# Performance work log

Hardware: AMD Instinct MI355X
Metric: run time of the kernel (lower is better)

Reference implementation:

```python
import jax, jax.numpy as jnp
import numpy as np

IN_F = 4096
OUT_F = 4096
B, S = 4, 2048
RMS_EPS = 1e-6
Q_EPS = 1e-5


def setup_inputs() -> dict:
    key = jax.random.key(0)
    kx, kw, kb, ks = jax.random.split(key, 4)
    x = jax.random.normal(kx, (B, S, IN_F), dtype=jnp.float32)
    # ternary BitNet weight in {-1, 0, +1}, stored as float32 for the reference
    W = (jax.random.randint(kw, (OUT_F, IN_F), 0, 3) - 1).astype(jnp.float32)
    rms_weight = jnp.ones((IN_F,), dtype=jnp.float32)
    bias = jax.random.normal(kb, (OUT_F,), dtype=jnp.float32)
    weight_scale = jax.random.uniform(ks, (1,), dtype=jnp.float32) + 0.5
    return {"x": x, "W": W, "rms_weight": rms_weight, "bias": bias,
            "weight_scale": weight_scale}


def reference(x, W, rms_weight, bias, weight_scale):
    # RMSNorm (self.rms_norm applied before quantized matmul)
    var = jnp.mean(x * x, axis=-1, keepdims=True)
    h = x * jax.lax.rsqrt(var + RMS_EPS) * rms_weight
    # BitNet act_quant: per-token absmax int8 quantization
    scale = 127.0 / jnp.clip(jnp.max(jnp.abs(h), axis=-1, keepdims=True), Q_EPS)  # [B,S,1]
    q = jnp.clip(jnp.round(h * scale), -128.0, 127.0)
    # ternary GEMV per token, then dequant
    y = jnp.einsum('bsk,ok->bso', q, W) / scale  # [B,S,OUT_F]
    y = y + bias
    y = y * weight_scale  # weight_scale_mode == 'multiply'
    return y
```

## Files before the change

kernel.cpp:

```cpp
#include <hip/hip_runtime.h>

#define IN_F 4096
#define OUT_F 4096
#define NTOK 8192
#define KDIM 4096

using i32x4 = __attribute__((ext_vector_type(4))) int;
using f32x4 = __attribute__((ext_vector_type(4))) float;

__device__ __forceinline__ void gload_lds16(const void* g, void* l) {
  __builtin_amdgcn_global_load_lds(
      (const __attribute__((address_space(1))) void*)g,
      (__attribute__((address_space(3))) void*)l, 16, 0, 0);
}

#define WAITV(n) asm volatile("s_waitcnt vmcnt(" #n ")" ::: "memory")
#define BAR() do { asm volatile("" ::: "memory"); __builtin_amdgcn_s_barrier(); \
                   asm volatile("" ::: "memory"); } while (0)

__global__ __launch_bounds__(256) void rmsq_kernel(
    const float* __restrict__ x, const float* __restrict__ rmsw,
    signed char* __restrict__ q, float* __restrict__ dscale) {
  const int tok = blockIdx.x;
  const int tid = threadIdx.x;
  const f32x4* xr = (const f32x4*)(x + (size_t)tok * IN_F);
  const f32x4* wr = (const f32x4*)rmsw;

  f32x4 v[4];
  float ss = 0.f;
#pragma unroll
  for (int c = 0; c < 4; ++c) {
    v[c] = xr[c * 256 + tid];
    ss += v[c].x * v[c].x + v[c].y * v[c].y + v[c].z * v[c].z + v[c].w * v[c].w;
  }

  __shared__ float red[4];
#pragma unroll
  for (int off = 32; off > 0; off >>= 1) ss += __shfl_down(ss, off, 64);
  const int wid = tid >> 6;
  if ((tid & 63) == 0) red[wid] = ss;
  __syncthreads();
  const float tot = red[0] + red[1] + red[2] + red[3];
  const float rinv = rsqrtf(tot * (1.0f / IN_F) + 1e-6f);

  f32x4 h[4];
  float amax = 0.f;
#pragma unroll
  for (int c = 0; c < 4; ++c) {
    f32x4 w = wr[c * 256 + tid];
    h[c].x = v[c].x * rinv * w.x;
    h[c].y = v[c].y * rinv * w.y;
    h[c].z = v[c].z * rinv * w.z;
    h[c].w = v[c].w * rinv * w.w;
    amax = fmaxf(amax, fabsf(h[c].x));
    amax = fmaxf(amax, fabsf(h[c].y));
    amax = fmaxf(amax, fabsf(h[c].z));
    amax = fmaxf(amax, fabsf(h[c].w));
  }

  __syncthreads();
#pragma unroll
  for (int off = 32; off > 0; off >>= 1)
    amax = fmaxf(amax, __shfl_down(amax, off, 64));
  if ((tid & 63) == 0) red[wid] = amax;
  __syncthreads();
  amax = fmaxf(fmaxf(red[0], red[1]), fmaxf(red[2], red[3]));
  amax = fmaxf(amax, 1e-5f);
  const float qs = 127.0f / amax;
  if (tid == 0) dscale[tok] = amax * (1.0f / 127.0f);

  uint* qo = (uint*)(q + (size_t)tok * IN_F);
#pragma unroll
  for (int c = 0; c < 4; ++c) {
    float r0 = fminf(fmaxf(rintf(h[c].x * qs), -128.f), 127.f);
    float r1 = fminf(fmaxf(rintf(h[c].y * qs), -128.f), 127.f);
    float r2 = fminf(fmaxf(rintf(h[c].z * qs), -128.f), 127.f);
    float r3 = fminf(fmaxf(rintf(h[c].w * qs), -128.f), 127.f);
    uint p = ((uint)((int)r0 & 255)) | ((uint)((int)r1 & 255) << 8) |
             ((uint)((int)r2 & 255) << 16) | ((uint)((int)r3 & 255) << 24);
    qo[c * 256 + tid] = p;
  }
}

__global__ __launch_bounds__(256) void wconv_kernel(
    const float* __restrict__ W, signed char* __restrict__ Wq) {
  const int idx = blockIdx.x * 256 + threadIdx.x;
  f32x4 w = ((const f32x4*)W)[idx];
  uint p = ((uint)((int)w.x & 255)) | ((uint)((int)w.y & 255) << 8) |
           ((uint)((int)w.z & 255) << 16) | ((uint)((int)w.w & 255) << 24);
  ((uint*)Wq)[idx] = p;
}

#define BM 256
#define BN 256
#define BK 64
#define NT (KDIM / BK)
#define TILEB (BM * BK)
#define BUFB (2 * TILEB)
#define NBUF 4

__global__ __launch_bounds__(512, 2) void gemm_kernel(
    const signed char* __restrict__ A, const signed char* __restrict__ Bw,
    const float* __restrict__ dscale, const float* __restrict__ bias,
    const float* __restrict__ wscale_p, float* __restrict__ out) {
  __shared__ __align__(16) signed char lds[NBUF * BUFB];

  const int tid = threadIdx.x;
  const int lane = tid & 63;
  const int wid = tid >> 6;
  const int wr = wid >> 2;
  const int wc = wid & 3;

  const int bid = blockIdx.x;
  const int swz = (bid & 7) * 64 + (bid >> 3);
  const int m0 = (swz & 31) * BM;
  const int n0 = (swz >> 5) * BN;

  const int cA0 = tid, cA1 = tid + 512;
  const int rA0 = cA0 >> 2, rA1 = cA1 >> 2;
  const int sA0 = (cA0 & 3) ^ ((rA0 >> 1) & 3);
  const int sA1 = (cA1 & 3) ^ ((rA1 >> 1) & 3);
  const signed char* agp0 = A + (size_t)(m0 + rA0) * KDIM + sA0 * 16;
  const signed char* agp1 = A + (size_t)(m0 + rA1) * KDIM + sA1 * 16;
  const signed char* bgp0 = Bw + (size_t)(n0 + rA0) * KDIM + sA0 * 16;
  const signed char* bgp1 = Bw + (size_t)(n0 + rA1) * KDIM + sA1 * 16;

#define STAGE_ALL(kt, bufoff)                                              \
  do {                                                                     \
    const int k0_ = (kt) * BK;                                             \
    signed char* lb_ = &lds[(bufoff)];                                     \
    gload_lds16(agp0 + k0_, lb_ + cA0 * 16);                               \
    gload_lds16(agp1 + k0_, lb_ + cA1 * 16);                               \
    gload_lds16(bgp0 + k0_, lb_ + TILEB + cA0 * 16);                       \
    gload_lds16(bgp1 + k0_, lb_ + TILEB + cA1 * 16);                       \
  } while (0)

  const int fr = lane & 15;
  const int ks = lane >> 4;
  int offA[8], offB[4];
#pragma unroll
  for (int mi = 0; mi < 8; ++mi) {
    const int row = wr * 128 + mi * 16 + fr;
    offA[mi] = row * BK + ((ks ^ ((row >> 1) & 3)) * 16);
  }
#pragma unroll
  for (int ni = 0; ni < 4; ++ni) {
    const int row = wc * 64 + ni * 16 + fr;
    offB[ni] = TILEB + row * BK + ((ks ^ ((row >> 1) & 3)) * 16);
  }

  i32x4 acc[8][4];
#pragma unroll
  for (int i = 0; i < 8; ++i)
#pragma unroll
    for (int j = 0; j < 4; ++j) acc[i][j] = (i32x4){0, 0, 0, 0};

  STAGE_ALL(0, 0);
  STAGE_ALL(1, BUFB);
  STAGE_ALL(2, 2 * BUFB);
  WAITV(8);
  BAR();

  int bufo = 0;
  int sbufo = 3 * BUFB;
  for (int t = 0; t < NT; ++t) {
    const signed char* bp = &lds[bufo];
    signed char* sb = &lds[sbufo];
    const int k3 = (t + 3) * BK;
    const bool more = (t + 3 < NT);

#pragma unroll
    for (int q = 0; q < 4; ++q) {
      const int mi0 = (q >> 1) * 4;
      const int ni0 = (q & 1) * 2;

      i32x4 af0 = *(const i32x4*)(bp + offA[mi0 + 0]);
      i32x4 af1 = *(const i32x4*)(bp + offA[mi0 + 1]);
      i32x4 af2 = *(const i32x4*)(bp + offA[mi0 + 2]);
      i32x4 af3 = *(const i32x4*)(bp + offA[mi0 + 3]);
      i32x4 bf0 = *(const i32x4*)(bp + offB[ni0 + 0]);
      i32x4 bf1 = *(const i32x4*)(bp + offB[ni0 + 1]);

      if (more) {
        if (q == 0)      gload_lds16(agp0 + k3, sb + cA0 * 16);
        else if (q == 1) gload_lds16(agp1 + k3, sb + cA1 * 16);
        else if (q == 2) gload_lds16(bgp0 + k3, sb + TILEB + cA0 * 16);
        else             gload_lds16(bgp1 + k3, sb + TILEB + cA1 * 16);
      }

      BAR();
      __builtin_amdgcn_s_setprio(1);
      acc[mi0 + 0][ni0 + 0] = __builtin_amdgcn_mfma_i32_16x16x64_i8(af0, bf0, acc[mi0 + 0][ni0 + 0], 0, 0, 0);
      acc[mi0 + 1][ni0 + 0] = __builtin_amdgcn_mfma_i32_16x16x64_i8(af1, bf0, acc[mi0 + 1][ni0 + 0], 0, 0, 0);
      acc[mi0 + 2][ni0 + 0] = __builtin_amdgcn_mfma_i32_16x16x64_i8(af2, bf0, acc[mi0 + 2][ni0 + 0], 0, 0, 0);
      acc[mi0 + 3][ni0 + 0] = __builtin_amdgcn_mfma_i32_16x16x64_i8(af3, bf0, acc[mi0 + 3][ni0 + 0], 0, 0, 0);
      acc[mi0 + 0][ni0 + 1] = __builtin_amdgcn_mfma_i32_16x16x64_i8(af0, bf1, acc[mi0 + 0][ni0 + 1], 0, 0, 0);
      acc[mi0 + 1][ni0 + 1] = __builtin_amdgcn_mfma_i32_16x16x64_i8(af1, bf1, acc[mi0 + 1][ni0 + 1], 0, 0, 0);
      acc[mi0 + 2][ni0 + 1] = __builtin_amdgcn_mfma_i32_16x16x64_i8(af2, bf1, acc[mi0 + 2][ni0 + 1], 0, 0, 0);
      acc[mi0 + 3][ni0 + 1] = __builtin_amdgcn_mfma_i32_16x16x64_i8(af3, bf1, acc[mi0 + 3][ni0 + 1], 0, 0, 0);
      __builtin_amdgcn_s_setprio(0);

      if (q == 3) {
        if (t < NT - 3)       WAITV(8);
        else if (t == NT - 3) WAITV(4);
        else if (t == NT - 2) WAITV(0);
      }
      BAR();
    }

    bufo += BUFB;  if (bufo == NBUF * BUFB) bufo = 0;
    sbufo += BUFB; if (sbufo == NBUF * BUFB) sbufo = 0;
  }

  const float wsc = wscale_p[0];
  const int rbase = (lane >> 4) * 4;
  float bv[4];
#pragma unroll
  for (int ni = 0; ni < 4; ++ni) bv[ni] = bias[n0 + wc * 64 + ni * 16 + fr];
#pragma unroll
  for (int mi = 0; mi < 8; ++mi) {
#pragma unroll
    for (int r = 0; r < 4; ++r) {
      const int m = m0 + wr * 128 + mi * 16 + rbase + r;
      const float ds = dscale[m];
      float* orow = out + (size_t)m * OUT_F + n0 + wc * 64;
#pragma unroll
      for (int ni = 0; ni < 4; ++ni) {
        orow[ni * 16 + fr] = ((float)acc[mi][ni][r] * ds + bv[ni]) * wsc;
      }
    }
  }
#undef STAGE_ALL
}

extern "C" void kernel_launch(void* const* d_in, const int* in_sizes, int n_in,
                              void* d_out, int out_size, void* d_ws, size_t ws_size,
                              hipStream_t stream) {
  const float* x = (const float*)d_in[0];
  const float* W = (const float*)d_in[1];
  const float* rmsw = (const float*)d_in[2];
  const float* bias = (const float*)d_in[3];
  const float* wscale = (const float*)d_in[4];
  float* out = (float*)d_out;

  signed char* q = (signed char*)d_ws;
  signed char* Wq = q + (size_t)NTOK * IN_F;
  float* dscale = (float*)(Wq + (size_t)OUT_F * IN_F);

  rmsq_kernel<<<NTOK, 256, 0, stream>>>(x, rmsw, q, dscale);
  wconv_kernel<<<(OUT_F * IN_F / 4) / 256, 256, 0, stream>>>(W, Wq);
  gemm_kernel<<<(NTOK / BM) * (OUT_F / BN), 512, 0, stream>>>(q, Wq, dscale,
                                                              bias, wscale, out);
}
```

Measured before the change: 208.6 us.

## Software-pipeline LDS fragment loads one quarter-step ahead of MFMAs

Restructures the GEMM main loop so the A/B fragments for the next quarter-step (including the first quarter of the next K tile) are read from LDS while the current eight MFMAs run, using register double-buffering. The two barriers per quarter are cut to one, placed before the reads, and the vmcnt waits are moved ahead of that barrier. A partial lgkmcnt wait lets the MFMAs proceed without waiting for the prefetched LDS reads to land. This aims to hide LDS latency behind matrix work, at the cost of more live registers at two-workgroup occupancy and subtle ordering requirements between async global-to-LDS writes and reads.

```diff
diff --git a/kernel.cpp b/kernel.cpp
--- a/kernel.cpp
+++ b/kernel.cpp
@@ -98,6 +98,7 @@
 #define TILEB (BM * BK)
 #define BUFB (2 * TILEB)
 #define NBUF 4
+#define LDSMASK (NBUF * BUFB - 1)
 
 __global__ __launch_bounds__(512, 2) void gemm_kernel(
     const signed char* __restrict__ A, const signed char* __restrict__ Bw,
@@ -160,26 +161,41 @@
   STAGE_ALL(2, 2 * BUFB);
   WAITV(8);
   BAR();
+  i32x4 a0 = *(const i32x4*)(lds + offA[0]);
+  i32x4 a1 = *(const i32x4*)(lds + offA[1]);
+  i32x4 a2 = *(const i32x4*)(lds + offA[2]);
+  i32x4 a3 = *(const i32x4*)(lds + offA[3]);
+  i32x4 b0v = *(const i32x4*)(lds + offB[0]);
+  i32x4 b1v = *(const i32x4*)(lds + offB[1]);
 
   int bufo = 0;
-  int sbufo = 3 * BUFB;
   for (int t = 0; t < NT; ++t) {
     const signed char* bp = &lds[bufo];
-    signed char* sb = &lds[sbufo];
+    const signed char* np = (t + 1 < NT) ? &lds[(bufo + BUFB) & LDSMASK] : bp;
+    signed char* sb = &lds[(bufo + 3 * BUFB) & LDSMASK];
     const int k3 = (t + 3) * BK;
     const bool more = (t + 3 < NT);
 
 #pragma unroll
     for (int q = 0; q < 4; ++q) {
-      const int mi0 = (q >> 1) * 4;
-      const int ni0 = (q & 1) * 2;
-
-      i32x4 af0 = *(const i32x4*)(bp + offA[mi0 + 0]);
-      i32x4 af1 = *(const i32x4*)(bp + offA[mi0 + 1]);
-      i32x4 af2 = *(const i32x4*)(bp + offA[mi0 + 2]);
-      i32x4 af3 = *(const i32x4*)(bp + offA[mi0 + 3]);
-      i32x4 bf0 = *(const i32x4*)(bp + offB[ni0 + 0]);
-      i32x4 bf1 = *(const i32x4*)(bp + offB[ni0 + 1]);
+      const int mi0 = (q >> 1) * 4, ni0 = (q & 1) * 2;
+      const int qn = (q + 1) & 3;
+      const int mi0n = (qn >> 1) * 4, ni0n = (qn & 1) * 2;
+      const signed char* rp = (q < 3) ? bp : np;
+
+      if (q == 3) {
+        if (t < NT - 3)       WAITV(7);
+        else if (t == NT - 3) WAITV(4);
+        else if (t == NT - 2) WAITV(0);
+      }
+      BAR();
+
+      i32x4 na0 = *(const i32x4*)(rp + offA[mi0n + 0]);
+      i32x4 na1 = *(const i32x4*)(rp + offA[mi0n + 1]);
+      i32x4 na2 = *(const i32x4*)(rp + offA[mi0n + 2]);
+      i32x4 na3 = *(const i32x4*)(rp + offA[mi0n + 3]);
+      i32x4 nb0 = *(const i32x4*)(rp + offB[ni0n + 0]);
+      i32x4 nb1 = *(const i32x4*)(rp + offB[ni0n + 1]);
 
       if (more) {
         if (q == 0)      gload_lds16(agp0 + k3, sb + cA0 * 16);
@@ -188,28 +204,23 @@
         else             gload_lds16(bgp1 + k3, sb + TILEB + cA1 * 16);
       }
 
-      BAR();
+      asm volatile("s_waitcnt lgkmcnt(6)" ::: "memory");
+
       __builtin_amdgcn_s_setprio(1);
-      acc[mi0 + 0][ni0 + 0] = __builtin_amdgcn_mfma_i32_16x16x64_i8(af0, bf0, acc[mi0 + 0][ni0 + 0], 0, 0, 0);
-      acc[mi0 + 1][ni0 + 0] = __builtin_amdgcn_mfma_i32_16x16x64_i8(af1, bf0, acc[mi0 + 1][ni0 + 0], 0, 0, 0);
-      acc[mi0 + 2][ni0 + 0] = __builtin_amdgcn_mfma_i32_16x16x64_i8(af2, bf0, acc[mi0 + 2][ni0 + 0], 0, 0, 0);
-      acc[mi0 + 3][ni0 + 0] = __builtin_amdgcn_mfma_i32_16x16x64_i8(af3, bf0, acc[mi0 + 3][ni0 + 0], 0, 0, 0);
-      acc[mi0 + 0][ni0 + 1] = __builtin_amdgcn_mfma_i32_16x16x64_i8(af0, bf1, acc[mi0 + 0][ni0 + 1], 0, 0, 0);
-      acc[mi0 + 1][ni0 + 1] = __builtin_amdgcn_mfma_i32_16x16x64_i8(af1, bf1, acc[mi0 + 1][ni0 + 1], 0, 0, 0);
-      acc[mi0 + 2][ni0 + 1] = __builtin_amdgcn_mfma_i32_16x16x64_i8(af2, bf1, acc[mi0 + 2][ni0 + 1], 0, 0, 0);
-      acc[mi0 + 3][ni0 + 1] = __builtin_amdgcn_mfma_i32_16x16x64_i8(af3, bf1, acc[mi0 + 3][ni0 + 1], 0, 0, 0);
+      acc[mi0 + 0][ni0 + 0] = __builtin_amdgcn_mfma_i32_16x16x64_i8(a0, b0v, acc[mi0 + 0][ni0 + 0], 0, 0, 0);
+      acc[mi0 + 1][ni0 + 0] = __builtin_amdgcn_mfma_i32_16x16x64_i8(a1, b0v, acc[mi0 + 1][ni0 + 0], 0, 0, 0);
+      acc[mi0 + 2][ni0 + 0] = __builtin_amdgcn_mfma_i32_16x16x64_i8(a2, b0v, acc[mi0 + 2][ni0 + 0], 0, 0, 0);
+      acc[mi0 + 3][ni0 + 0] = __builtin_amdgcn_mfma_i32_16x16x64_i8(a3, b0v, acc[mi0 + 3][ni0 + 0], 0, 0, 0);
+      acc[mi0 + 0][ni0 + 1] = __builtin_amdgcn_mfma_i32_16x16x64_i8(a0, b1v, acc[mi0 + 0][ni0 + 1], 0, 0, 0);
+      acc[mi0 + 1][ni0 + 1] = __builtin_amdgcn_mfma_i32_16x16x64_i8(a1, b1v, acc[mi0 + 1][ni0 + 1], 0, 0, 0);
+      acc[mi0 + 2][ni0 + 1] = __builtin_amdgcn_mfma_i32_16x16x64_i8(a2, b1v, acc[mi0 + 2][ni0 + 1], 0, 0, 0);
+      acc[mi0 + 3][ni0 + 1] = __builtin_amdgcn_mfma_i32_16x16x64_i8(a3, b1v, acc[mi0 + 3][ni0 + 1], 0, 0, 0);
       __builtin_amdgcn_s_setprio(0);
 
-      if (q == 3) {
-        if (t < NT - 3)       WAITV(8);
-        else if (t == NT - 3) WAITV(4);
-        else if (t == NT - 2) WAITV(0);
-      }
-      BAR();
+      a0 = na0; a1 = na1; a2 = na2; a3 = na3; b0v = nb0; b1v = nb1;
     }
 
-    bufo += BUFB;  if (bufo == NBUF * BUFB) bufo = 0;
-    sbufo += BUFB; if (sbufo == NBUF * BUFB) sbufo = 0;
+    bufo = (bufo + BUFB) & LDSMASK;
   }
 
   const float wsc = wscale_p[0];
```

Result: faster. 196.5 us (-5.8%).
